# Optimization experiments

Hardware: AMD Instinct MI355X
Metric: run time of the kernel (lower is better)

The kernel has to match this reference:

```python
import jax, jax.numpy as jnp
import numpy as np

EPS_DEPTH = 0.001  # validity threshold from target_points.ge(0.001)
BIG = 1e10         # stands in for masked-out (padded) y points


def setup_inputs() -> dict:
    key = jax.random.key(0)
    k1, k2 = jax.random.split(key)
    L, N, P1 = 4, 4, 257          # n_scales, batch, n_bin_edges (256 bins)
    H, W = 240, 320
    bins = jax.random.uniform(k1, (L, N, P1), dtype=jnp.float32)
    target_depth_maps = jax.random.uniform(k2, (N, H, W), dtype=jnp.float32)
    return {"bins": bins, "target_depth_maps": target_depth_maps}


def _chamfer_1d(centers, y, mask, y_lengths):
    # centers: [N, P] bin centers; y: [N, M] flattened depths; mask: [N, M] valid
    # squared pairwise distances in 1-D: [N, P, M]
    d = (centers[:, :, None] - y[:, None, :]) ** 2
    # x -> y: min over VALID y points, mean over P bin centers
    dx = jnp.where(mask[:, None, :], d, BIG)
    cham_x = dx.min(axis=2).mean(axis=1)                       # [N]
    # y -> x: min over bin centers, sum over valid y / y_length
    dy = jnp.where(mask, d.min(axis=1), 0.0)                   # [N, M]
    cham_y = dy.sum(axis=1) / y_lengths                        # [N]
    return (cham_x + cham_y).mean()  # batch_reduction="mean"


def reference(bins, target_depth_maps):
    N = target_depth_maps.shape[0]
    y = target_depth_maps.reshape(N, -1)                       # [N, M]
    mask = y >= EPS_DEPTH                                      # ragged validity mask
    y_lengths = mask.sum(axis=1).astype(y.dtype)               # [N]
    loss = jnp.zeros((), dtype=y.dtype)
    for bin_edges in bins:  # fixed small loop over scales (multi=True)
        centers = 0.5 * (bin_edges[:, 1:] + bin_edges[:, :-1])  # [N, P]
        loss = loss + _chamfer_1d(centers, y, mask, y_lengths)
    return loss
```

## Files before the change

kernel.cpp:

```cpp
#include <hip/hip_runtime.h>


#define NSCALES 4
#define NBATCH  4
#define NEDGES  257
#define NP      256
#define NM      76800
#define CHUNK   256
#define NCHUNK  (NM / CHUNK)
#define BLOCK   256
#define NLN     (NSCALES * NBATCH)
#define BIGF    1e10f

__global__ __launch_bounds__(BLOCK) void bcl_init(float* __restrict__ minabs,
                                                  float* __restrict__ sumy,
                                                  unsigned int* __restrict__ cnt) {
    const int t = blockIdx.x * BLOCK + threadIdx.x;
    if (t < NLN * NP) minabs[t] = BIGF;
    if (t < NLN)      sumy[t]   = 0.0f;
    if (t < NBATCH)   cnt[t]    = 0u;
}

__global__ __launch_bounds__(BLOCK) void bcl_main(const float* __restrict__ bins,
                                                  const float* __restrict__ depth,
                                                  float* __restrict__ minabs,
                                                  float* __restrict__ sumy,
                                                  unsigned int* __restrict__ cnt) {
    __shared__ float sY[CHUNK];
    __shared__ float sC[NSCALES * NP];
    __shared__ float redS[BLOCK / 64][NSCALES];
    __shared__ unsigned int redC[BLOCK / 64];

    const int b = blockIdx.x;
    const int n = b / NCHUNK;
    const int chunk = b - n * NCHUNK;
    const int t = threadIdx.x;

    {
        const float v = depth[n * NM + chunk * CHUNK + t];
        sY[t] = (v >= 0.001f) ? v : 3e9f;
    }
#pragma unroll
    for (int k = 0; k < 4; ++k) {
        const int i = t + k * BLOCK;
        const int l = i >> 8;
        const int p = i & (NP - 1);
        const float* e = bins + (l * NBATCH + n) * NEDGES + p;
        sC[i] = 0.5f * (e[0] + e[1]);
    }
    __syncthreads();

    float ca[NSCALES], ma[NSCALES];
#pragma unroll
    for (int l = 0; l < NSCALES; ++l) { ca[l] = sC[t + (l << 8)]; ma[l] = BIGF; }

    const float4* sY4 = (const float4*)sY;
#pragma unroll 4
    for (int q = 0; q < CHUNK / 4; ++q) {
        const float4 y4 = sY4[q];
#pragma unroll
        for (int l = 0; l < NSCALES; ++l) {
            ma[l] = fminf(fminf(ma[l], fabsf(ca[l] - y4.x)), fabsf(ca[l] - y4.y));
            ma[l] = fminf(fminf(ma[l], fabsf(ca[l] - y4.z)), fabsf(ca[l] - y4.w));
        }
    }
#pragma unroll
    for (int l = 0; l < NSCALES; ++l) {
        const int idx = (l * NBATCH + n) * NP + t;
        if (ma[l] < minabs[idx])
            atomicMin((int*)(minabs + idx), __float_as_int(ma[l]));
    }

    const float y = sY[t];
    const bool valid = (y < 2.0f);

    float suml[NSCALES];
    const float4* sC4 = (const float4*)sC;
#pragma unroll
    for (int l = 0; l < NSCALES; ++l) {
        float m = BIGF;
#pragma unroll 4
        for (int q = 0; q < NP / 4; ++q) {
            const float4 c = sC4[(l << 6) + q];
            m = fminf(fminf(m, fabsf(c.x - y)), fabsf(c.y - y));
            m = fminf(fminf(m, fabsf(c.z - y)), fabsf(c.w - y));
        }
        suml[l] = valid ? m * m : 0.0f;
    }
    unsigned int cc = valid ? 1u : 0u;

#pragma unroll
    for (int off = 32; off; off >>= 1) {
#pragma unroll
        for (int l = 0; l < NSCALES; ++l) suml[l] += __shfl_down(suml[l], off);
        cc += __shfl_down(cc, off);
    }
    const int wv = t >> 6;
    if ((t & 63) == 0) {
#pragma unroll
        for (int l = 0; l < NSCALES; ++l) redS[wv][l] = suml[l];
        redC[wv] = cc;
    }
    __syncthreads();
    if (t < NSCALES) {
        const float s = redS[0][t] + redS[1][t] + redS[2][t] + redS[3][t];
        atomicAdd(&sumy[t * NBATCH + n], s);
    }
    if (t == 0) {
        const unsigned int c4 = redC[0] + redC[1] + redC[2] + redC[3];
        atomicAdd(&cnt[n], c4);
    }
}

__global__ __launch_bounds__(BLOCK) void bcl_final(const float* __restrict__ minabs,
                                                   const float* __restrict__ sumy,
                                                   const unsigned int* __restrict__ cnt,
                                                   float* __restrict__ out) {
    __shared__ float red[BLOCK / 64];
    const int t = threadIdx.x;
    float s = 0.0f;
#pragma unroll
    for (int k = 0; k < (NLN * NP) / BLOCK; ++k) {
        const float m = minabs[t + k * BLOCK];
        s += m * m;
    }
#pragma unroll
    for (int off = 32; off; off >>= 1) s += __shfl_down(s, off);
    if ((t & 63) == 0) red[t >> 6] = s;
    __syncthreads();
    if (t == 0) {
        const float S = red[0] + red[1] + red[2] + red[3];
        float lossB = 0.0f;
#pragma unroll
        for (int i = 0; i < NLN; ++i)
            lossB += sumy[i] / (float)cnt[i & (NBATCH - 1)];
        out[0] = (S / (float)NP + lossB) / (float)NBATCH;
    }
}

extern "C" void kernel_launch(void* const* d_in, const int* in_sizes, int n_in,
                              void* d_out, int out_size, void* d_ws, size_t ws_size,
                              hipStream_t stream) {
    const float* bins  = (const float*)d_in[0];
    const float* depth = (const float*)d_in[1];

    float* minabs = (float*)d_ws;
    float* sumy   = minabs + NLN * NP;
    unsigned int* cnt = (unsigned int*)(sumy + NLN);

    bcl_init <<<NLN * NP / BLOCK, BLOCK, 0, stream>>>(minabs, sumy, cnt);
    bcl_main <<<NBATCH * NCHUNK,  BLOCK, 0, stream>>>(bins, depth, minabs, sumy, cnt);
    bcl_final<<<1,                BLOCK, 0, stream>>>(minabs, sumy, cnt, (float*)d_out);
}
```

Baseline: 105.3 us.

## Precompute centers and masked depths in prep kernel; stream from global instead of LDS

A new prep kernel computes the bin centers and the sentinel-masked depth values once into workspace, replacing the init kernel. The main kernel then drops its shared-memory staging and __syncthreads, and reads y and center values as wave-uniform loads straight from global memory (likely scalar loads) in 16-wide register windows. This removes redundant center computation per block and the LDS traffic. In exchange it adds an extra pass that writes the full depth array to global memory and relies on cache hits for the repeated uniform loads.

New measurement: 105.1 us. Within noise of the previous version (-0.2%).

```diff
diff --git a/kernel.cpp b/kernel.cpp
--- a/kernel.cpp
+++ b/kernel.cpp
@@ -11,23 +11,43 @@
 #define BLOCK   256
 #define NLN     (NSCALES * NBATCH)
 #define BIGF    1e10f
+#define SENT    3e9f
 
-__global__ __launch_bounds__(BLOCK) void bcl_init(float* __restrict__ minabs,
-                                                  float* __restrict__ sumy,
-                                                  unsigned int* __restrict__ cnt) {
-    const int t = blockIdx.x * BLOCK + threadIdx.x;
-    if (t < NLN * NP) minabs[t] = BIGF;
-    if (t < NLN)      sumy[t]   = 0.0f;
-    if (t < NBATCH)   cnt[t]    = 0u;
+#define WS_MIN   0
+#define WS_SUMY  4096
+#define WS_CNT   4112
+#define WS_CENT  4352
+#define WS_Y     8448
+
+__global__ __launch_bounds__(BLOCK) void bcl_prep(const float* __restrict__ bins,
+                                                  const float* __restrict__ depth,
+                                                  float* __restrict__ ws) {
+    const int b = blockIdx.x;
+    const int t = threadIdx.x;
+    if (b < NLN) {
+        const float* e = bins + b * NEDGES;
+        ws[WS_CENT + b * NP + t] = 0.5f * (e[t] + e[t + 1]);
+        ws[WS_MIN + b * NP + t] = BIGF;
+        if (b == 0) {
+            if (t < NLN)    ws[WS_SUMY + t] = 0.0f;
+            if (t < NBATCH) ((unsigned int*)ws)[WS_CNT + t] = 0u;
+        }
+    } else {
+        const int base = (b - NLN) * 1024 + t * 4;
+        float4 v = *(const float4*)(depth + base);
+        v.x = (v.x >= 0.001f) ? v.x : SENT;
+        v.y = (v.y >= 0.001f) ? v.y : SENT;
+        v.z = (v.z >= 0.001f) ? v.z : SENT;
+        v.w = (v.w >= 0.001f) ? v.w : SENT;
+        *(float4*)(ws + WS_Y + base) = v;
+    }
 }
 
-__global__ __launch_bounds__(BLOCK) void bcl_main(const float* __restrict__ bins,
-                                                  const float* __restrict__ depth,
+__global__ __launch_bounds__(BLOCK) void bcl_main(const float* __restrict__ cent,
+                                                  const float* __restrict__ yarr,
                                                   float* __restrict__ minabs,
                                                   float* __restrict__ sumy,
                                                   unsigned int* __restrict__ cnt) {
-    __shared__ float sY[CHUNK];
-    __shared__ float sC[NSCALES * NP];
     __shared__ float redS[BLOCK / 64][NSCALES];
     __shared__ unsigned int redC[BLOCK / 64];
 
@@ -36,55 +56,61 @@
     const int chunk = b - n * NCHUNK;
     const int t = threadIdx.x;
 
-    {
-        const float v = depth[n * NM + chunk * CHUNK + t];
-        sY[t] = (v >= 0.001f) ? v : 3e9f;
-    }
+    float ca[NSCALES];
 #pragma unroll
-    for (int k = 0; k < 4; ++k) {
-        const int i = t + k * BLOCK;
-        const int l = i >> 8;
-        const int p = i & (NP - 1);
-        const float* e = bins + (l * NBATCH + n) * NEDGES + p;
-        sC[i] = 0.5f * (e[0] + e[1]);
-    }
-    __syncthreads();
+    for (int l = 0; l < NSCALES; ++l)
+        ca[l] = cent[(l * NBATCH + n) * NP + t];
+    const float yv = yarr[n * NM + chunk * CHUNK + t];
+    const bool valid = (yv < 2.0f);
 
-    float ca[NSCALES], ma[NSCALES];
+    const float* __restrict__ ystream = yarr + n * NM + chunk * CHUNK;
+    float ma[NSCALES];
 #pragma unroll
-    for (int l = 0; l < NSCALES; ++l) { ca[l] = sC[t + (l << 8)]; ma[l] = BIGF; }
+    for (int l = 0; l < NSCALES; ++l) ma[l] = BIGF;
 
-    const float4* sY4 = (const float4*)sY;
-#pragma unroll 4
-    for (int q = 0; q < CHUNK / 4; ++q) {
-        const float4 y4 = sY4[q];
+#pragma unroll 2
+    for (int w = 0; w < CHUNK / 16; ++w) {
+        float yw[16];
 #pragma unroll
-        for (int l = 0; l < NSCALES; ++l) {
-            ma[l] = fminf(fminf(ma[l], fabsf(ca[l] - y4.x)), fabsf(ca[l] - y4.y));
-            ma[l] = fminf(fminf(ma[l], fabsf(ca[l] - y4.z)), fabsf(ca[l] - y4.w));
+        for (int j = 0; j < 16; ++j) yw[j] = ystream[w * 16 + j];
+#pragma unroll
+        for (int j = 0; j < 16; j += 2) {
+#pragma unroll
+            for (int l = 0; l < NSCALES; ++l) {
+                const float d0 = ca[l] - yw[j];
+                const float d1 = ca[l] - yw[j + 1];
+                ma[l] = fminf(fminf(ma[l], fabsf(d0)), fabsf(d1));
+            }
         }
     }
 #pragma unroll
     for (int l = 0; l < NSCALES; ++l) {
         const int idx = (l * NBATCH + n) * NP + t;
         if (ma[l] < minabs[idx])
-            atomicMin((int*)(minabs + idx), __float_as_int(ma[l]));
+            atomicMin((int*)minabs + idx, __float_as_int(ma[l]));
     }
 
-    const float y = sY[t];
-    const bool valid = (y < 2.0f);
-
     float suml[NSCALES];
-    const float4* sC4 = (const float4*)sC;
 #pragma unroll
     for (int l = 0; l < NSCALES; ++l) {
-        float m = BIGF;
-#pragma unroll 4
-        for (int q = 0; q < NP / 4; ++q) {
-            const float4 c = sC4[(l << 6) + q];
-            m = fminf(fminf(m, fabsf(c.x - y)), fabsf(c.y - y));
-            m = fminf(fminf(m, fabsf(c.z - y)), fabsf(c.w - y));
+        const float* __restrict__ cstream = cent + (l * NBATCH + n) * NP;
+        float m0 = BIGF, m1 = BIGF;
+#pragma unroll 2
+        for (int w = 0; w < NP / 16; ++w) {
+            float cw[16];
+#pragma unroll
+            for (int j = 0; j < 16; ++j) cw[j] = cstream[w * 16 + j];
+#pragma unroll
+            for (int j = 0; j < 16; j += 4) {
+                const float d0 = cw[j]     - yv;
+                const float d1 = cw[j + 1] - yv;
+                const float d2 = cw[j + 2] - yv;
+                const float d3 = cw[j + 3] - yv;
+                m0 = fminf(fminf(m0, fabsf(d0)), fabsf(d1));
+                m1 = fminf(fminf(m1, fabsf(d2)), fabsf(d3));
+            }
         }
+        const float m = fminf(m0, m1);
         suml[l] = valid ? m * m : 0.0f;
     }
     unsigned int cc = valid ? 1u : 0u;
@@ -112,16 +138,14 @@
     }
 }
 
-__global__ __launch_bounds__(BLOCK) void bcl_final(const float* __restrict__ minabs,
-                                                   const float* __restrict__ sumy,
-                                                   const unsigned int* __restrict__ cnt,
+__global__ __launch_bounds__(BLOCK) void bcl_final(const float* __restrict__ ws,
                                                    float* __restrict__ out) {
     __shared__ float red[BLOCK / 64];
     const int t = threadIdx.x;
     float s = 0.0f;
 #pragma unroll
-    for (int k = 0; k < (NLN * NP) / BLOCK; ++k) {
-        const float m = minabs[t + k * BLOCK];
+    for (int k = 0; k < NLN; ++k) {
+        const float m = ws[WS_MIN + t + k * BLOCK];
         s += m * m;
     }
 #pragma unroll
@@ -133,7 +157,8 @@
         float lossB = 0.0f;
 #pragma unroll
         for (int i = 0; i < NLN; ++i)
-            lossB += sumy[i] / (float)cnt[i & (NBATCH - 1)];
+            lossB += ws[WS_SUMY + i] /
+                     (float)((const unsigned int*)ws)[WS_CNT + (i & (NBATCH - 1))];
         out[0] = (S / (float)NP + lossB) / (float)NBATCH;
     }
 }
@@ -143,12 +168,11 @@
                               hipStream_t stream) {
     const float* bins  = (const float*)d_in[0];
     const float* depth = (const float*)d_in[1];
+    float* ws = (float*)d_ws;
 
-    float* minabs = (float*)d_ws;
-    float* sumy   = minabs + NLN * NP;
-    unsigned int* cnt = (unsigned int*)(sumy + NLN);
-
-    bcl_init <<<NLN * NP / BLOCK, BLOCK, 0, stream>>>(minabs, sumy, cnt);
-    bcl_main <<<NBATCH * NCHUNK,  BLOCK, 0, stream>>>(bins, depth, minabs, sumy, cnt);
-    bcl_final<<<1,                BLOCK, 0, stream>>>(minabs, sumy, cnt, (float*)d_out);
+    bcl_prep <<<NLN + NM * NBATCH / 1024, BLOCK, 0, stream>>>(bins, depth, ws);
+    bcl_main <<<NBATCH * NCHUNK, BLOCK, 0, stream>>>(
+        ws + WS_CENT, ws + WS_Y, ws + WS_MIN, ws + WS_SUMY,
+        (unsigned int*)ws + WS_CNT);
+    bcl_final<<<1, BLOCK, 0, stream>>>(ws, (float*)d_out);
 }
```

## Replace shared-memory chunk scan with per-wave register rotation via ds_bpermute

Applied to the files above, without the earlier changes.

Each wavefront now processes 64 depth points against all 256 bin centres held in registers (4 per lane per scale). Y values and running y-side minima rotate around the wave with ds_bpermute, so every computed distance updates both the x-side and the y-side minimum. This removes the separate second pass over centres, the shared-memory staging and the block barriers. The costs are more atomicMin traffic (every lane issues 16 atomics per wave, no early-out check), many more blocks, and cross-lane permute latency on every step.

Result: slower. 317.5 us (+201.4%).

```diff
diff --git a/kernel.cpp b/kernel.cpp
--- a/kernel.cpp
+++ b/kernel.cpp
@@ -6,19 +6,26 @@
 #define NEDGES  257
 #define NP      256
 #define NM      76800
-#define CHUNK   256
-#define NCHUNK  (NM / CHUNK)
 #define BLOCK   256
+#define WPN     (NM / 64)
+#define NBLK    (NBATCH * WPN / 4)
 #define NLN     (NSCALES * NBATCH)
 #define BIGF    1e10f
+#define SENT    3e9f
 
-__global__ __launch_bounds__(BLOCK) void bcl_init(float* __restrict__ minabs,
-                                                  float* __restrict__ sumy,
-                                                  unsigned int* __restrict__ cnt) {
+#define WS_MIN  0
+#define WS_SUMY 4096
+#define WS_CNT  4112
+
+__global__ __launch_bounds__(BLOCK) void bcl_init(float* __restrict__ ws) {
     const int t = blockIdx.x * BLOCK + threadIdx.x;
-    if (t < NLN * NP) minabs[t] = BIGF;
-    if (t < NLN)      sumy[t]   = 0.0f;
-    if (t < NBATCH)   cnt[t]    = 0u;
+    if (t < NLN * NP) ws[WS_MIN + t] = BIGF;
+    if (t < NLN)      ws[WS_SUMY + t] = 0.0f;
+    if (t < NBATCH)   ((unsigned int*)ws)[WS_CNT + t] = 0u;
+}
+
+__device__ __forceinline__ float rot1(float v, int pidx) {
+    return __int_as_float(__builtin_amdgcn_ds_bpermute(pidx, __float_as_int(v)));
 }
 
 __global__ __launch_bounds__(BLOCK) void bcl_main(const float* __restrict__ bins,
@@ -26,89 +33,81 @@
                                                   float* __restrict__ minabs,
                                                   float* __restrict__ sumy,
                                                   unsigned int* __restrict__ cnt) {
-    __shared__ float sY[CHUNK];
-    __shared__ float sC[NSCALES * NP];
-    __shared__ float redS[BLOCK / 64][NSCALES];
-    __shared__ unsigned int redC[BLOCK / 64];
+    const int lane = threadIdx.x & 63;
+    const int wv   = threadIdx.x >> 6;
+    const int gw   = blockIdx.x * 4 + wv;
+    const int n    = gw / WPN;
+    const int yg   = gw - n * WPN;
 
-    const int b = blockIdx.x;
-    const int n = b / NCHUNK;
-    const int chunk = b - n * NCHUNK;
-    const int t = threadIdx.x;
+    float ca[NSCALES][4], ma[NSCALES][4];
+#pragma unroll
+    for (int l = 0; l < NSCALES; ++l) {
+        const float* e = bins + (l * NBATCH + n) * NEDGES;
+#pragma unroll
+        for (int k = 0; k < 4; ++k) {
+            const int p = lane + 64 * k;
+            ca[l][k] = 0.5f * (e[p] + e[p + 1]);
+            ma[l][k] = BIGF;
+        }
+    }
 
-    {
-        const float v = depth[n * NM + chunk * CHUNK + t];
-        sY[t] = (v >= 0.001f) ? v : 3e9f;
-    }
+    const float yraw = depth[n * NM + yg * 64 + lane];
+    const bool valid = (yraw >= 0.001f);
+    float y = valid ? yraw : SENT;
+    float mb[NSCALES];
 #pragma unroll
-    for (int k = 0; k < 4; ++k) {
-        const int i = t + k * BLOCK;
-        const int l = i >> 8;
-        const int p = i & (NP - 1);
-        const float* e = bins + (l * NBATCH + n) * NEDGES + p;
-        sC[i] = 0.5f * (e[0] + e[1]);
-    }
-    __syncthreads();
+    for (int l = 0; l < NSCALES; ++l) mb[l] = BIGF;
 
-    float ca[NSCALES], ma[NSCALES];
+    const int pidx = ((lane + 63) & 63) * 4;
+
+#pragma unroll 2
+    for (int it = 0; it < 32; ++it) {
+        y = rot1(y, pidx);
 #pragma unroll
-    for (int l = 0; l < NSCALES; ++l) { ca[l] = sC[t + (l << 8)]; ma[l] = BIGF; }
-
-    const float4* sY4 = (const float4*)sY;
-#pragma unroll 4
-    for (int q = 0; q < CHUNK / 4; ++q) {
-        const float4 y4 = sY4[q];
+        for (int l = 0; l < NSCALES; ++l) mb[l] = rot1(mb[l], pidx);
+        float dA[NSCALES][4];
 #pragma unroll
         for (int l = 0; l < NSCALES; ++l) {
-            ma[l] = fminf(fminf(ma[l], fabsf(ca[l] - y4.x)), fabsf(ca[l] - y4.y));
-            ma[l] = fminf(fminf(ma[l], fabsf(ca[l] - y4.z)), fabsf(ca[l] - y4.w));
+#pragma unroll
+            for (int k = 0; k < 4; ++k) dA[l][k] = ca[l][k] - y;
+            mb[l] = fminf(fminf(mb[l], fabsf(dA[l][0])), fabsf(dA[l][1]));
+            mb[l] = fminf(fminf(mb[l], fabsf(dA[l][2])), fabsf(dA[l][3]));
+        }
+        y = rot1(y, pidx);
+#pragma unroll
+        for (int l = 0; l < NSCALES; ++l) mb[l] = rot1(mb[l], pidx);
+#pragma unroll
+        for (int l = 0; l < NSCALES; ++l) {
+            const float dB0 = ca[l][0] - y, dB1 = ca[l][1] - y;
+            const float dB2 = ca[l][2] - y, dB3 = ca[l][3] - y;
+            mb[l] = fminf(fminf(mb[l], fabsf(dB0)), fabsf(dB1));
+            mb[l] = fminf(fminf(mb[l], fabsf(dB2)), fabsf(dB3));
+            ma[l][0] = fminf(fminf(ma[l][0], fabsf(dA[l][0])), fabsf(dB0));
+            ma[l][1] = fminf(fminf(ma[l][1], fabsf(dA[l][1])), fabsf(dB1));
+            ma[l][2] = fminf(fminf(ma[l][2], fabsf(dA[l][2])), fabsf(dB2));
+            ma[l][3] = fminf(fminf(ma[l][3], fabsf(dA[l][3])), fabsf(dB3));
         }
     }
+
 #pragma unroll
-    for (int l = 0; l < NSCALES; ++l) {
-        const int idx = (l * NBATCH + n) * NP + t;
-        if (ma[l] < minabs[idx])
-            atomicMin((int*)(minabs + idx), __float_as_int(ma[l]));
-    }
-
-    const float y = sY[t];
-    const bool valid = (y < 2.0f);
+    for (int l = 0; l < NSCALES; ++l)
+#pragma unroll
+        for (int k = 0; k < 4; ++k)
+            atomicMin(((int*)minabs) + (l * NBATCH + n) * NP + lane + 64 * k,
+                      __float_as_int(ma[l][k]));
 
     float suml[NSCALES];
-    const float4* sC4 = (const float4*)sC;
 #pragma unroll
-    for (int l = 0; l < NSCALES; ++l) {
-        float m = BIGF;
-#pragma unroll 4
-        for (int q = 0; q < NP / 4; ++q) {
-            const float4 c = sC4[(l << 6) + q];
-            m = fminf(fminf(m, fabsf(c.x - y)), fabsf(c.y - y));
-            m = fminf(fminf(m, fabsf(c.z - y)), fabsf(c.w - y));
-        }
-        suml[l] = valid ? m * m : 0.0f;
-    }
-    unsigned int cc = valid ? 1u : 0u;
-
+    for (int l = 0; l < NSCALES; ++l) suml[l] = valid ? mb[l] * mb[l] : 0.0f;
 #pragma unroll
-    for (int off = 32; off; off >>= 1) {
+    for (int off = 32; off; off >>= 1)
 #pragma unroll
         for (int l = 0; l < NSCALES; ++l) suml[l] += __shfl_down(suml[l], off);
-        cc += __shfl_down(cc, off);
-    }
-    const int wv = t >> 6;
-    if ((t & 63) == 0) {
+    const unsigned long long bal = __ballot(valid);
+    if (lane == 0) {
 #pragma unroll
-        for (int l = 0; l < NSCALES; ++l) redS[wv][l] = suml[l];
-        redC[wv] = cc;
-    }
-    __syncthreads();
-    if (t < NSCALES) {
-        const float s = redS[0][t] + redS[1][t] + redS[2][t] + redS[3][t];
-        atomicAdd(&sumy[t * NBATCH + n], s);
-    }
-    if (t == 0) {
-        const unsigned int c4 = redC[0] + redC[1] + redC[2] + redC[3];
-        atomicAdd(&cnt[n], c4);
+        for (int l = 0; l < NSCALES; ++l) atomicAdd(&sumy[l * NBATCH + n], suml[l]);
+        atomicAdd(&cnt[n], (unsigned int)__popcll(bal));
     }
 }
 
@@ -120,7 +119,7 @@
     const int t = threadIdx.x;
     float s = 0.0f;
 #pragma unroll
-    for (int k = 0; k < (NLN * NP) / BLOCK; ++k) {
+    for (int k = 0; k < NLN; ++k) {
         const float m = minabs[t + k * BLOCK];
         s += m * m;
     }
@@ -143,12 +142,13 @@
                               hipStream_t stream) {
     const float* bins  = (const float*)d_in[0];
     const float* depth = (const float*)d_in[1];
+    float* ws = (float*)d_ws;
 
-    float* minabs = (float*)d_ws;
-    float* sumy   = minabs + NLN * NP;
-    unsigned int* cnt = (unsigned int*)(sumy + NLN);
+    float* minabs = ws + WS_MIN;
+    float* sumy   = ws + WS_SUMY;
+    unsigned int* cnt = (unsigned int*)ws + WS_CNT;
 
-    bcl_init <<<NLN * NP / BLOCK, BLOCK, 0, stream>>>(minabs, sumy, cnt);
-    bcl_main <<<NBATCH * NCHUNK,  BLOCK, 0, stream>>>(bins, depth, minabs, sumy, cnt);
+    bcl_init <<<NLN * NP / BLOCK, BLOCK, 0, stream>>>(ws);
+    bcl_main <<<NBLK,             BLOCK, 0, stream>>>(bins, depth, minabs, sumy, cnt);
     bcl_final<<<1,                BLOCK, 0, stream>>>(minabs, sumy, cnt, (float*)d_out);
 }
```

## Split chamfer main kernel into separate x->y and y->x kernels with register blocking

Applied to the files above, without the earlier changes.

Splits the fused main kernel into two. One computes the per-bin minimum over chunks of depth points, with the bin centers held in registers. The other computes the per-point minimum over bin centers, with each thread handling four points for one scale, and the grid spread across scales and point groups. Both inner loops software-prefetch the next float4 from shared memory. The aim is more parallelism and lower register and shared-memory pressure per block, at the cost of an extra kernel launch and reading the depth map twice.

After: 119.2 us. 1.13x slower.

```diff
diff --git a/kernel.cpp b/kernel.cpp
--- a/kernel.cpp
+++ b/kernel.cpp
@@ -6,122 +6,148 @@
 #define NEDGES  257
 #define NP      256
 #define NM      76800
-#define CHUNK   256
-#define NCHUNK  (NM / CHUNK)
 #define BLOCK   256
+#define ACHUNK  256
+#define ANCH    (NM / ACHUNK)
+#define BGRP    1024
+#define BNG     (NM / BGRP)
 #define NLN     (NSCALES * NBATCH)
 #define BIGF    1e10f
+#define SENT    3e9f
 
-__global__ __launch_bounds__(BLOCK) void bcl_init(float* __restrict__ minabs,
-                                                  float* __restrict__ sumy,
-                                                  unsigned int* __restrict__ cnt) {
+#define WS_MIN  0
+#define WS_SUMY 4096
+#define WS_CNT  4112
+
+__global__ __launch_bounds__(BLOCK) void bcl_init(float* __restrict__ ws) {
     const int t = blockIdx.x * BLOCK + threadIdx.x;
-    if (t < NLN * NP) minabs[t] = BIGF;
-    if (t < NLN)      sumy[t]   = 0.0f;
-    if (t < NBATCH)   cnt[t]    = 0u;
+    if (t < NLN * NP) ws[WS_MIN + t] = BIGF;
+    if (t < NLN)      ws[WS_SUMY + t] = 0.0f;
+    if (t < NBATCH)   ((unsigned int*)ws)[WS_CNT + t] = 0u;
 }
 
-__global__ __launch_bounds__(BLOCK) void bcl_main(const float* __restrict__ bins,
-                                                  const float* __restrict__ depth,
-                                                  float* __restrict__ minabs,
-                                                  float* __restrict__ sumy,
-                                                  unsigned int* __restrict__ cnt) {
-    __shared__ float sY[CHUNK];
-    __shared__ float sC[NSCALES * NP];
-    __shared__ float redS[BLOCK / 64][NSCALES];
-    __shared__ unsigned int redC[BLOCK / 64];
-
+__global__ __launch_bounds__(BLOCK) void bcl_a(const float* __restrict__ bins,
+                                               const float* __restrict__ depth,
+                                               float* __restrict__ minabs) {
+    __shared__ float sY[ACHUNK];
     const int b = blockIdx.x;
-    const int n = b / NCHUNK;
-    const int chunk = b - n * NCHUNK;
+    const int n = b / ANCH;
+    const int chunk = b - n * ANCH;
     const int t = threadIdx.x;
 
     {
-        const float v = depth[n * NM + chunk * CHUNK + t];
-        sY[t] = (v >= 0.001f) ? v : 3e9f;
+        const float v = depth[n * NM + chunk * ACHUNK + t];
+        sY[t] = (v >= 0.001f) ? v : SENT;
     }
+    float ca[NSCALES], ma[NSCALES];
 #pragma unroll
-    for (int k = 0; k < 4; ++k) {
-        const int i = t + k * BLOCK;
-        const int l = i >> 8;
-        const int p = i & (NP - 1);
-        const float* e = bins + (l * NBATCH + n) * NEDGES + p;
-        sC[i] = 0.5f * (e[0] + e[1]);
+    for (int l = 0; l < NSCALES; ++l) {
+        const float* e = bins + (l * NBATCH + n) * NEDGES + t;
+        ca[l] = 0.5f * (e[0] + e[1]);
+        ma[l] = BIGF;
     }
     __syncthreads();
 
-    float ca[NSCALES], ma[NSCALES];
-#pragma unroll
-    for (int l = 0; l < NSCALES; ++l) { ca[l] = sC[t + (l << 8)]; ma[l] = BIGF; }
-
     const float4* sY4 = (const float4*)sY;
+    float4 cur = sY4[0];
 #pragma unroll 4
-    for (int q = 0; q < CHUNK / 4; ++q) {
-        const float4 y4 = sY4[q];
+    for (int w = 0; w < ACHUNK / 4 - 1; ++w) {
+        const float4 nxt = sY4[w + 1];
 #pragma unroll
         for (int l = 0; l < NSCALES; ++l) {
-            ma[l] = fminf(fminf(ma[l], fabsf(ca[l] - y4.x)), fabsf(ca[l] - y4.y));
-            ma[l] = fminf(fminf(ma[l], fabsf(ca[l] - y4.z)), fabsf(ca[l] - y4.w));
+            ma[l] = fminf(fminf(ma[l], fabsf(ca[l] - cur.x)), fabsf(ca[l] - cur.y));
+            ma[l] = fminf(fminf(ma[l], fabsf(ca[l] - cur.z)), fabsf(ca[l] - cur.w));
         }
+        cur = nxt;
+    }
+#pragma unroll
+    for (int l = 0; l < NSCALES; ++l) {
+        ma[l] = fminf(fminf(ma[l], fabsf(ca[l] - cur.x)), fabsf(ca[l] - cur.y));
+        ma[l] = fminf(fminf(ma[l], fabsf(ca[l] - cur.z)), fabsf(ca[l] - cur.w));
     }
 #pragma unroll
     for (int l = 0; l < NSCALES; ++l) {
         const int idx = (l * NBATCH + n) * NP + t;
         if (ma[l] < minabs[idx])
-            atomicMin((int*)(minabs + idx), __float_as_int(ma[l]));
+            atomicMin((int*)minabs + idx, __float_as_int(ma[l]));
     }
+}
 
-    const float y = sY[t];
-    const bool valid = (y < 2.0f);
+__global__ __launch_bounds__(BLOCK) void bcl_b(const float* __restrict__ bins,
+                                               const float* __restrict__ depth,
+                                               float* __restrict__ sumy,
+                                               unsigned int* __restrict__ cnt) {
+    __shared__ float sC[NP];
+    __shared__ float redS[BLOCK / 64];
+    __shared__ unsigned int redC[BLOCK / 64];
+    const int b = blockIdx.x;
+    const int n = b / (NSCALES * BNG);
+    const int r = b - n * (NSCALES * BNG);
+    const int l = r / BNG;
+    const int g = r - l * BNG;
+    const int t = threadIdx.x;
 
-    float suml[NSCALES];
+    {
+        const float* e = bins + (l * NBATCH + n) * NEDGES + t;
+        sC[t] = 0.5f * (e[0] + e[1]);
+    }
+    const float4 yv = *(const float4*)(depth + n * NM + g * BGRP + t * 4);
+    const bool v0 = yv.x >= 0.001f, v1 = yv.y >= 0.001f;
+    const bool v2 = yv.z >= 0.001f, v3 = yv.w >= 0.001f;
+    float m0 = BIGF, m1 = BIGF, m2 = BIGF, m3 = BIGF;
+    __syncthreads();
+
     const float4* sC4 = (const float4*)sC;
-#pragma unroll
-    for (int l = 0; l < NSCALES; ++l) {
-        float m = BIGF;
+    float4 cur = sC4[0];
 #pragma unroll 4
-        for (int q = 0; q < NP / 4; ++q) {
-            const float4 c = sC4[(l << 6) + q];
-            m = fminf(fminf(m, fabsf(c.x - y)), fabsf(c.y - y));
-            m = fminf(fminf(m, fabsf(c.z - y)), fabsf(c.w - y));
-        }
-        suml[l] = valid ? m * m : 0.0f;
+    for (int w = 0; w < NP / 4 - 1; ++w) {
+        const float4 nxt = sC4[w + 1];
+        m0 = fminf(fminf(m0, fabsf(cur.x - yv.x)), fabsf(cur.y - yv.x));
+        m0 = fminf(fminf(m0, fabsf(cur.z - yv.x)), fabsf(cur.w - yv.x));
+        m1 = fminf(fminf(m1, fabsf(cur.x - yv.y)), fabsf(cur.y - yv.y));
+        m1 = fminf(fminf(m1, fabsf(cur.z - yv.y)), fabsf(cur.w - yv.y));
+        m2 = fminf(fminf(m2, fabsf(cur.x - yv.z)), fabsf(cur.y - yv.z));
+        m2 = fminf(fminf(m2, fabsf(cur.z - yv.z)), fabsf(cur.w - yv.z));
+        m3 = fminf(fminf(m3, fabsf(cur.x - yv.w)), fabsf(cur.y - yv.w));
+        m3 = fminf(fminf(m3, fabsf(cur.z - yv.w)), fabsf(cur.w - yv.w));
+        cur = nxt;
     }
-    unsigned int cc = valid ? 1u : 0u;
+    m0 = fminf(fminf(m0, fabsf(cur.x - yv.x)), fabsf(cur.y - yv.x));
+    m0 = fminf(fminf(m0, fabsf(cur.z - yv.x)), fabsf(cur.w - yv.x));
+    m1 = fminf(fminf(m1, fabsf(cur.x - yv.y)), fabsf(cur.y - yv.y));
+    m1 = fminf(fminf(m1, fabsf(cur.z - yv.y)), fabsf(cur.w - yv.y));
+    m2 = fminf(fminf(m2, fabsf(cur.x - yv.z)), fabsf(cur.y - yv.z));
+    m2 = fminf(fminf(m2, fabsf(cur.z - yv.z)), fabsf(cur.w - yv.z));
+    m3 = fminf(fminf(m3, fabsf(cur.x - yv.w)), fabsf(cur.y - yv.w));
+    m3 = fminf(fminf(m3, fabsf(cur.z - yv.w)), fabsf(cur.w - yv.w));
+
+    float suml = (v0 ? m0 * m0 : 0.0f) + (v1 ? m1 * m1 : 0.0f)
+               + (v2 ? m2 * m2 : 0.0f) + (v3 ? m3 * m3 : 0.0f);
+    unsigned int cc = (v0 ? 1u : 0u) + (v1 ? 1u : 0u) + (v2 ? 1u : 0u) + (v3 ? 1u : 0u);
 
 #pragma unroll
     for (int off = 32; off; off >>= 1) {
-#pragma unroll
-        for (int l = 0; l < NSCALES; ++l) suml[l] += __shfl_down(suml[l], off);
-        cc += __shfl_down(cc, off);
+        suml += __shfl_down(suml, off);
+        cc   += __shfl_down(cc, off);
     }
     const int wv = t >> 6;
-    if ((t & 63) == 0) {
-#pragma unroll
-        for (int l = 0; l < NSCALES; ++l) redS[wv][l] = suml[l];
-        redC[wv] = cc;
-    }
+    if ((t & 63) == 0) { redS[wv] = suml; redC[wv] = cc; }
     __syncthreads();
-    if (t < NSCALES) {
-        const float s = redS[0][t] + redS[1][t] + redS[2][t] + redS[3][t];
-        atomicAdd(&sumy[t * NBATCH + n], s);
-    }
     if (t == 0) {
-        const unsigned int c4 = redC[0] + redC[1] + redC[2] + redC[3];
-        atomicAdd(&cnt[n], c4);
+        atomicAdd(&sumy[l * NBATCH + n], redS[0] + redS[1] + redS[2] + redS[3]);
+        if (l == 0)
+            atomicAdd(&cnt[n], redC[0] + redC[1] + redC[2] + redC[3]);
     }
 }
 
-__global__ __launch_bounds__(BLOCK) void bcl_final(const float* __restrict__ minabs,
-                                                   const float* __restrict__ sumy,
-                                                   const unsigned int* __restrict__ cnt,
+__global__ __launch_bounds__(BLOCK) void bcl_final(const float* __restrict__ ws,
                                                    float* __restrict__ out) {
     __shared__ float red[BLOCK / 64];
     const int t = threadIdx.x;
     float s = 0.0f;
 #pragma unroll
-    for (int k = 0; k < (NLN * NP) / BLOCK; ++k) {
-        const float m = minabs[t + k * BLOCK];
+    for (int k = 0; k < NLN; ++k) {
+        const float m = ws[WS_MIN + t + k * BLOCK];
         s += m * m;
     }
 #pragma unroll
@@ -133,7 +159,8 @@
         float lossB = 0.0f;
 #pragma unroll
         for (int i = 0; i < NLN; ++i)
-            lossB += sumy[i] / (float)cnt[i & (NBATCH - 1)];
+            lossB += ws[WS_SUMY + i] /
+                     (float)((const unsigned int*)ws)[WS_CNT + (i & (NBATCH - 1))];
         out[0] = (S / (float)NP + lossB) / (float)NBATCH;
     }
 }
@@ -143,12 +170,14 @@
                               hipStream_t stream) {
     const float* bins  = (const float*)d_in[0];
     const float* depth = (const float*)d_in[1];
+    float* ws = (float*)d_ws;
 
-    float* minabs = (float*)d_ws;
-    float* sumy   = minabs + NLN * NP;
-    unsigned int* cnt = (unsigned int*)(sumy + NLN);
+    float* minabs = ws + WS_MIN;
+    float* sumy   = ws + WS_SUMY;
+    unsigned int* cnt = (unsigned int*)ws + WS_CNT;
 
-    bcl_init <<<NLN * NP / BLOCK, BLOCK, 0, stream>>>(minabs, sumy, cnt);
-    bcl_main <<<NBATCH * NCHUNK,  BLOCK, 0, stream>>>(bins, depth, minabs, sumy, cnt);
-    bcl_final<<<1,                BLOCK, 0, stream>>>(minabs, sumy, cnt, (float*)d_out);
+    bcl_init <<<NLN * NP / BLOCK,       BLOCK, 0, stream>>>(ws);
+    bcl_a    <<<NBATCH * ANCH,          BLOCK, 0, stream>>>(bins, depth, minabs);
+    bcl_b    <<<NBATCH * NSCALES * BNG, BLOCK, 0, stream>>>(bins, depth, sumy, cnt);
+    bcl_final<<<1,                      BLOCK, 0, stream>>>(ws, (float*)d_out);
 }
```
